# Performance work log

Measured on AMD Instinct MI355X. Metric: run time of the kernel, lower is better.

## Reference

```python
import jax, jax.numpy as jnp
import numpy as np

H = 10          # hidden_size
TAIL = 1440     # slice out[:, -1440:-1, :]


def _cell(x, h, c, w_ih, w_hh, b):
    # PyTorch LSTM gate order: i, f, g, o
    gates = x @ w_ih.T + h @ w_hh.T + b          # [B, 4H]
    i, f, g, o = jnp.split(gates, 4, axis=-1)
    c = jax.nn.sigmoid(f) * c + jax.nn.sigmoid(i) * jnp.tanh(g)
    h = jax.nn.sigmoid(o) * jnp.tanh(c)
    return h, c


def setup_inputs() -> dict:
    key = jax.random.key(0)
    ks = jax.random.split(key, 13)
    s = 1.0 / np.sqrt(H)  # PyTorch default init range

    def u(k, shape):
        return jax.random.uniform(k, shape, jnp.float32, -s, s)

    return {
        "x": jax.random.normal(ks[0], (4096, 2048), jnp.float32),
        "w_ih0": u(ks[1], (4 * H, 1)),
        "w_hh0": u(ks[2], (4 * H, H)),
        "b_ih0": u(ks[3], (4 * H,)),
        "b_hh0": u(ks[4], (4 * H,)),
        "w_ih1": u(ks[5], (4 * H, H)),
        "w_hh1": u(ks[6], (4 * H, H)),
        "b_ih1": u(ks[7], (4 * H,)),
        "b_hh1": u(ks[8], (4 * H,)),
        "fc1_w": u(ks[9], (6, H)),
        "fc1_b": u(ks[10], (6,)),
        "fc2_w": u(ks[11], (1, 6)),
        "fc2_b": u(ks[12], (1,)),
    }


def reference(x, w_ih0, w_hh0, b_ih0, b_hh0, w_ih1, w_hh1, b_ih1, b_hh1,
              fc1_w, fc1_b, fc2_w, fc2_b):
    B, T = x.shape
    xt = x[..., None].transpose(1, 0, 2)         # [T, B, 1] time-major
    b0 = b_ih0 + b_hh0
    b1 = b_ih1 + b_hh1
    z = jnp.zeros((B, H), x.dtype)

    def step(carry, xi):
        h0, c0, h1, c1 = carry
        h0, c0 = _cell(xi, h0, c0, w_ih0, w_hh0, b0)
        h1, c1 = _cell(h0, h1, c1, w_ih1, w_hh1, b1)
        return (h0, c0, h1, c1), h1

    _, ys = jax.lax.scan(step, (z, z, z, z), xt)  # ys: [T, B, H]
    out = ys.transpose(1, 0, 2)[:, T - TAIL:T - 1, :]   # [B, 1439, H]
    out = jnp.tanh(out @ fc1_w.T + fc1_b)                # [B, 1439, 6]
    out = out @ fc2_w.T + fc2_b                          # [B, 1439, 1]
    return out[..., 0]                                   # [B, 1439]
```

## Files before the change

### kernel.cpp

```cpp
#include <hip/hip_runtime.h>

typedef float v2f __attribute__((ext_vector_type(2)));

#define T_LEN 2048
#define NH    10
#define OUT_T 1439
#define TFIRST 608
#define NSEQ  4096
#define CH    16
#define NCH   (T_LEN / CH)
#define MFIRST (TFIRST / CH)

#define KSIG (-1.4426950408889634f)
#define KTAN (-2.8853900817779268f)

static __device__ __forceinline__ v2f fma2(v2f a, v2f b, v2f c) {
  return __builtin_elementwise_fma(a, b, c);
}
static __device__ __forceinline__ v2f splat2(float v) { v2f r; r.x = v; r.y = v; return r; }
static __device__ __forceinline__ v2f mulsp(v2f a, float s) { v2f r; r.x = a.x*s; r.y = a.y*s; return r; }
static __device__ __forceinline__ float rcp1p(float e) {
  return __builtin_amdgcn_rcpf(1.0f + e);
}

#define ROR_F(v, N) __uint_as_float(__builtin_amdgcn_update_dpp( \
    0, (int)__float_as_uint(v), 0x120 + (N), 0xF, 0xF, true))

__global__ void __launch_bounds__(128, 2)
lstm_fused(const float* __restrict__ x,
           const float* __restrict__ w_ih0, const float* __restrict__ w_hh0,
           const float* __restrict__ b_ih0, const float* __restrict__ b_hh0,
           const float* __restrict__ w_ih1, const float* __restrict__ w_hh1,
           const float* __restrict__ b_ih1, const float* __restrict__ b_hh1,
           const float* __restrict__ fc1_w, const float* __restrict__ fc1_b,
           const float* __restrict__ fc2_w, const float* __restrict__ fc2_b,
           float* __restrict__ out)
{
  __shared__ __align__(16) float h0buf[2][CH][64];
  __shared__ __align__(16) float h1buf[2][CH][64];

  const int tid  = threadIdx.x;
  const int wid  = tid >> 6;
  const int lane = tid & 63;
  const int grp  = lane >> 4;
  const int u    = lane & 15;
  const int seq  = (int)blockIdx.x * 4 + grp;

  v2f wIF[NH], wGO[NH], vIF[NH], vGO[NH];
  v2f wx_if, wx_go, bb_if, bb_go;
  wx_if = wx_go = bb_if = bb_go = splat2(0.f);
#pragma unroll
  for (int j = 0; j < NH; ++j) {
    wIF[j] = splat2(0.f); wGO[j] = splat2(0.f);
    vIF[j] = splat2(0.f); vGO[j] = splat2(0.f);
  }
  float fcw[NH];
#pragma unroll
  for (int j = 0; j < NH; ++j) fcw[j] = 0.f;
  float fcb = 0.f, fc2w2 = 0.f, fc2wn = 0.f;
  const float fc2bl = fc2_b[0];

  if (wid == 0) {
    if (u < NH) {
      const int ri = 0*NH+u, rf = 1*NH+u, rg = 2*NH+u, ro = 3*NH+u;
      wx_if.x = KSIG * w_ih0[ri];            wx_if.y = KSIG * w_ih0[rf];
      wx_go.x = KTAN * w_ih0[rg];            wx_go.y = KSIG * w_ih0[ro];
      bb_if.x = KSIG * (b_ih0[ri] + b_hh0[ri]); bb_if.y = KSIG * (b_ih0[rf] + b_hh0[rf]);
      bb_go.x = KTAN * (b_ih0[rg] + b_hh0[rg]); bb_go.y = KSIG * (b_ih0[ro] + b_hh0[ro]);
#pragma unroll
      for (int j = 0; j < NH; ++j) {
        wIF[j].x = KSIG * w_hh0[ri*NH+j]; wIF[j].y = KSIG * w_hh0[rf*NH+j];
        wGO[j].x = KTAN * w_hh0[rg*NH+j]; wGO[j].y = KSIG * w_hh0[ro*NH+j];
      }
    }
    if (u < 6) {
      fcb = KTAN * fc1_b[u];
      const float w2 = fc2_w[u];
      fc2w2 = 2.f * w2; fc2wn = -w2;
#pragma unroll
      for (int j = 0; j < NH; ++j) fcw[j] = KTAN * fc1_w[u*NH + j];
    }
  } else {
    if (u < NH) {
      const int ri = 0*NH+u, rf = 1*NH+u, rg = 2*NH+u, ro = 3*NH+u;
      bb_if.x = KSIG * (b_ih1[ri] + b_hh1[ri]); bb_if.y = KSIG * (b_ih1[rf] + b_hh1[rf]);
      bb_go.x = KTAN * (b_ih1[rg] + b_hh1[rg]); bb_go.y = KSIG * (b_ih1[ro] + b_hh1[ro]);
#pragma unroll
      for (int j = 0; j < NH; ++j) {
        wIF[j].x = KSIG * w_ih1[ri*NH+j]; wIF[j].y = KSIG * w_ih1[rf*NH+j];
        wGO[j].x = KTAN * w_ih1[rg*NH+j]; wGO[j].y = KSIG * w_ih1[ro*NH+j];
        vIF[j].x = KSIG * w_hh1[ri*NH+j]; vIF[j].y = KSIG * w_hh1[rf*NH+j];
        vGO[j].x = KTAN * w_hh1[rg*NH+j]; vGO[j].y = KSIG * w_hh1[ro*NH+j];
      }
    }
  }

  const float* xp   = x + (size_t)seq * T_LEN;
  float*       outp = out + (size_t)seq * OUT_T;

  float c = 0.f;
  float r0=0.f,r1=0.f,r2=0.f,r3=0.f,r4=0.f,r5=0.f,r6=0.f,r7=0.f,r8=0.f,r9=0.f;

  auto a_chunk = [&](int m) {
    float* hb = &h0buf[m & 1][0][0];
    const float* hr = &h0buf[m & 1][0][grp * 16];
    const float4* xq = (const float4*)(xp + m * CH);
    float4 xw[CH / 4];
#pragma unroll
    for (int i = 0; i < CH / 4; ++i) xw[i] = xq[i];
#pragma unroll
    for (int s = 0; s < CH; ++s) {
      const float xv = ((const float*)xw)[s];
      v2f aA = fma2(wx_if, splat2(xv), bb_if);
      v2f gA = fma2(wx_go, splat2(xv), bb_go);
      v2f aB = mulsp(wIF[1], r1);
      v2f gB = mulsp(wGO[1], r1);
#define L0T(j, hv, AC, GC) { const v2f sp = splat2(hv); \
      AC = fma2(wIF[j], sp, AC); GC = fma2(wGO[j], sp, GC); }
      L0T(0,r0,aA,gA) L0T(2,r2,aA,gA) L0T(3,r3,aB,gB) L0T(4,r4,aA,gA)
      L0T(5,r5,aB,gB) L0T(6,r6,aA,gA) L0T(7,r7,aB,gB) L0T(8,r8,aA,gA)
      L0T(9,r9,aB,gB)
#undef L0T
      const v2f gif = aA + aB;
      const v2f ggo = gA + gB;
      const float si = rcp1p(__builtin_amdgcn_exp2f(gif.x));
      const float sf = rcp1p(__builtin_amdgcn_exp2f(gif.y));
      const float rg = rcp1p(__builtin_amdgcn_exp2f(ggo.x));
      const float so = rcp1p(__builtin_amdgcn_exp2f(ggo.y));
      const float tgp = __builtin_fmaf(rg, 2.f*KTAN, -KTAN);
      c = __builtin_fmaf(sf, c, si * tgp);
      const float rc = rcp1p(__builtin_amdgcn_exp2f(c));
      const float tc = __builtin_fmaf(rc, 2.f, -1.f);
      const float h0n = so * tc;
      hb[s*64 + lane] = h0n;
      const float4 va = *(const float4*)(hr + s*64);
      const float4 vb = *(const float4*)(hr + s*64 + 4);
      const float2 vc = *(const float2*)(hr + s*64 + 8);
      r0=va.x; r1=va.y; r2=va.z; r3=va.w;
      r4=vb.x; r5=vb.y; r6=vb.z; r7=vb.w;
      r8=vc.x; r9=vc.y;
    }
  };

  auto b_chunk = [&](int m) {
    const float* hbi = &h0buf[m & 1][0][grp * 16];
    float* ob = &h1buf[m & 1][0][0];
    const float* orr = &h1buf[m & 1][0][grp * 16];
#pragma unroll
    for (int s = 0; s < CH; ++s) {
      const float4 pa = *(const float4*)(hbi + s*64);
      const float4 pb = *(const float4*)(hbi + s*64 + 4);
      const float2 pc = *(const float2*)(hbi + s*64 + 8);
      v2f cA = fma2(wIF[0], splat2(pa.x), bb_if);
      v2f hA = fma2(wGO[0], splat2(pa.x), bb_go);
      v2f cB = mulsp(wIF[1], pa.y);
      v2f hB = mulsp(wGO[1], pa.y);
#define L1I(j, hv, AC, GC) { const v2f sp = splat2(hv); \
      AC = fma2(wIF[j], sp, AC); GC = fma2(wGO[j], sp, GC); }
      L1I(2,pa.z,cA,hA) L1I(3,pa.w,cB,hB) L1I(4,pb.x,cA,hA) L1I(5,pb.y,cB,hB)
      L1I(6,pb.z,cA,hA) L1I(7,pb.w,cB,hB) L1I(8,pc.x,cA,hA) L1I(9,pc.y,cB,hB)
#undef L1I
      v2f cC = mulsp(vIF[0], r0);
      v2f hC = mulsp(vGO[0], r0);
      v2f cD = mulsp(vIF[1], r1);
      v2f hD = mulsp(vGO[1], r1);
#define L1R(j, hv, AC, GC) { const v2f sp = splat2(hv); \
      AC = fma2(vIF[j], sp, AC); GC = fma2(vGO[j], sp, GC); }
      L1R(2,r2,cC,hC) L1R(3,r3,cD,hD) L1R(4,r4,cC,hC) L1R(5,r5,cD,hD)
      L1R(6,r6,cC,hC) L1R(7,r7,cD,hD) L1R(8,r8,cC,hC) L1R(9,r9,cD,hD)
#undef L1R
      const v2f gif = (cA + cB) + (cC + cD);
      const v2f ggo = (hA + hB) + (hC + hD);
      const float si = rcp1p(__builtin_amdgcn_exp2f(gif.x));
      const float sf = rcp1p(__builtin_amdgcn_exp2f(gif.y));
      const float rg = rcp1p(__builtin_amdgcn_exp2f(ggo.x));
      const float so = rcp1p(__builtin_amdgcn_exp2f(ggo.y));
      const float tgp = __builtin_fmaf(rg, 2.f*KTAN, -KTAN);
      c = __builtin_fmaf(sf, c, si * tgp);
      const float rc = rcp1p(__builtin_amdgcn_exp2f(c));
      const float tc = __builtin_fmaf(rc, 2.f, -1.f);
      const float h1n = so * tc;
      ob[s*64 + lane] = h1n;
      const float4 va = *(const float4*)(orr + s*64);
      const float4 vb = *(const float4*)(orr + s*64 + 4);
      const float2 vc = *(const float2*)(orr + s*64 + 8);
      r0=va.x; r1=va.y; r2=va.z; r3=va.w;
      r4=vb.x; r5=vb.y; r6=vb.z; r7=vb.w;
      r8=vc.x; r9=vc.y;
    }
  };

  auto fc_chunk = [&](int m) {
    const float* hb = &h1buf[m & 1][0][grp * 16];
    float* oq = outp + (m * CH - TFIRST);
#pragma unroll
    for (int s = 0; s < CH; ++s) {
      if (m * CH + s < TFIRST + OUT_T) {
        const float4 pa = *(const float4*)(hb + s*64);
        const float4 pb = *(const float4*)(hb + s*64 + 4);
        const float2 pc = *(const float2*)(hb + s*64 + 8);
        float acc = __builtin_fmaf(pa.x, fcw[0], fcb);
        acc = __builtin_fmaf(pa.y, fcw[1], acc);
        acc = __builtin_fmaf(pa.z, fcw[2], acc);
        acc = __builtin_fmaf(pa.w, fcw[3], acc);
        acc = __builtin_fmaf(pb.x, fcw[4], acc);
        acc = __builtin_fmaf(pb.y, fcw[5], acc);
        acc = __builtin_fmaf(pb.z, fcw[6], acc);
        acc = __builtin_fmaf(pb.w, fcw[7], acc);
        acc = __builtin_fmaf(pc.x, fcw[8], acc);
        acc = __builtin_fmaf(pc.y, fcw[9], acc);
        const float rc = rcp1p(__builtin_amdgcn_exp2f(acc));
        float y = __builtin_fmaf(rc, fc2w2, fc2wn);
        y += ROR_F(y, 8);
        y += ROR_F(y, 4);
        y += ROR_F(y, 2);
        y += ROR_F(y, 1);
        if (u == 0) oq[s] = y + fc2bl;
      }
    }
  };

#pragma unroll 1
  for (int r = 0; r < NCH + 2; ++r) {
    if (wid == 0) {
      if (r < NCH) a_chunk(r);
      const int m = r - 2;
      if (m >= MFIRST && m < NCH) fc_chunk(m);
    } else {
      if (r >= 1 && r <= NCH) b_chunk(r - 1);
    }
    __syncthreads();
  }
}

extern "C" void kernel_launch(void* const* d_in, const int* in_sizes, int n_in,
                              void* d_out, int out_size, void* d_ws, size_t ws_size,
                              hipStream_t stream) {
  const float* x     = (const float*)d_in[0];
  const float* w_ih0 = (const float*)d_in[1];
  const float* w_hh0 = (const float*)d_in[2];
  const float* b_ih0 = (const float*)d_in[3];
  const float* b_hh0 = (const float*)d_in[4];
  const float* w_ih1 = (const float*)d_in[5];
  const float* w_hh1 = (const float*)d_in[6];
  const float* b_ih1 = (const float*)d_in[7];
  const float* b_hh1 = (const float*)d_in[8];
  const float* fc1_w = (const float*)d_in[9];
  const float* fc1_b = (const float*)d_in[10];
  const float* fc2_w = (const float*)d_in[11];
  const float* fc2_b = (const float*)d_in[12];
  float* out = (float*)d_out;

  lstm_fused<<<dim3(NSEQ / 4), dim3(128), 0, stream>>>(
      x, w_ih0, w_hh0, b_ih0, b_hh0, w_ih1, w_hh1, b_ih1, b_hh1,
      fc1_w, fc1_b, fc2_w, fc2_b, out);
}
```

Before: 724.0 us.

## Broadcast recurrent hidden state via ds_swizzle, double chunk size, partially unroll

Within each recurrent step, the new hidden values are now broadcast across the lanes of each 16-lane group with ds_swizzle broadcasts, replacing the previous write-then-read through shared memory. Chunk length doubles from 16 to 32 steps, halving the number of block-wide barriers. Loops change from full unroll to 4-step bodies to keep code size and registers in check. The risk is that ten swizzles per step may cost as much as the LDS reads, and the reduced unrolling may hurt scheduling.

```diff
diff --git a/kernel.cpp b/kernel.cpp
--- a/kernel.cpp
+++ b/kernel.cpp
@@ -7,7 +7,7 @@
 #define OUT_T 1439
 #define TFIRST 608
 #define NSEQ  4096
-#define CH    16
+#define CH    32
 #define NCH   (T_LEN / CH)
 #define MFIRST (TFIRST / CH)
 
@@ -22,6 +22,9 @@
 static __device__ __forceinline__ float rcp1p(float e) {
   return __builtin_amdgcn_rcpf(1.0f + e);
 }
+
+#define SWZB(v, j) __uint_as_float(__builtin_amdgcn_ds_swizzle( \
+    (int)__float_as_uint(v), (((j) << 5) | 0x10)))
 
 #define ROR_F(v, N) __uint_as_float(__builtin_amdgcn_update_dpp( \
     0, (int)__float_as_uint(v), 0x120 + (N), 0xF, 0xF, true))
@@ -101,121 +104,133 @@
   float c = 0.f;
   float r0=0.f,r1=0.f,r2=0.f,r3=0.f,r4=0.f,r5=0.f,r6=0.f,r7=0.f,r8=0.f,r9=0.f;
 
+  auto l0_step = [&](float xv, float* dst) {
+    v2f aA = fma2(wx_if, splat2(xv), bb_if);
+    v2f gA = fma2(wx_go, splat2(xv), bb_go);
+    v2f aB = mulsp(wIF[1], r1);
+    v2f gB = mulsp(wGO[1], r1);
+#define L0T(j, hv) { const v2f sp = splat2(hv); \
+    ((j & 1) ? aB : aA) = fma2(wIF[j], sp, ((j & 1) ? aB : aA)); \
+    ((j & 1) ? gB : gA) = fma2(wGO[j], sp, ((j & 1) ? gB : gA)); }
+    L0T(0,r0) L0T(2,r2) L0T(3,r3) L0T(4,r4) L0T(5,r5)
+    L0T(6,r6) L0T(7,r7) L0T(8,r8) L0T(9,r9)
+#undef L0T
+    const v2f gif = aA + aB;
+    const v2f ggo = gA + gB;
+    const float si = rcp1p(__builtin_amdgcn_exp2f(gif.x));
+    const float sf = rcp1p(__builtin_amdgcn_exp2f(gif.y));
+    const float rg = rcp1p(__builtin_amdgcn_exp2f(ggo.x));
+    const float so = rcp1p(__builtin_amdgcn_exp2f(ggo.y));
+    const float tgp = __builtin_fmaf(rg, 2.f*KTAN, -KTAN);
+    c = __builtin_fmaf(sf, c, si * tgp);
+    const float rc = rcp1p(__builtin_amdgcn_exp2f(c));
+    const float tc = __builtin_fmaf(rc, 2.f, -1.f);
+    const float h0n = so * tc;
+    *dst = h0n;
+    r0 = SWZB(h0n,0); r1 = SWZB(h0n,1); r2 = SWZB(h0n,2); r3 = SWZB(h0n,3);
+    r4 = SWZB(h0n,4); r5 = SWZB(h0n,5); r6 = SWZB(h0n,6); r7 = SWZB(h0n,7);
+    r8 = SWZB(h0n,8); r9 = SWZB(h0n,9);
+  };
+
   auto a_chunk = [&](int m) {
-    float* hb = &h0buf[m & 1][0][0];
-    const float* hr = &h0buf[m & 1][0][grp * 16];
+    float* hb = &h0buf[m & 1][0][0] + lane;
     const float4* xq = (const float4*)(xp + m * CH);
-    float4 xw[CH / 4];
-#pragma unroll
-    for (int i = 0; i < CH / 4; ++i) xw[i] = xq[i];
-#pragma unroll
-    for (int s = 0; s < CH; ++s) {
-      const float xv = ((const float*)xw)[s];
-      v2f aA = fma2(wx_if, splat2(xv), bb_if);
-      v2f gA = fma2(wx_go, splat2(xv), bb_go);
-      v2f aB = mulsp(wIF[1], r1);
-      v2f gB = mulsp(wGO[1], r1);
-#define L0T(j, hv, AC, GC) { const v2f sp = splat2(hv); \
-      AC = fma2(wIF[j], sp, AC); GC = fma2(wGO[j], sp, GC); }
-      L0T(0,r0,aA,gA) L0T(2,r2,aA,gA) L0T(3,r3,aB,gB) L0T(4,r4,aA,gA)
-      L0T(5,r5,aB,gB) L0T(6,r6,aA,gA) L0T(7,r7,aB,gB) L0T(8,r8,aA,gA)
-      L0T(9,r9,aB,gB)
-#undef L0T
-      const v2f gif = aA + aB;
-      const v2f ggo = gA + gB;
-      const float si = rcp1p(__builtin_amdgcn_exp2f(gif.x));
-      const float sf = rcp1p(__builtin_amdgcn_exp2f(gif.y));
-      const float rg = rcp1p(__builtin_amdgcn_exp2f(ggo.x));
-      const float so = rcp1p(__builtin_amdgcn_exp2f(ggo.y));
-      const float tgp = __builtin_fmaf(rg, 2.f*KTAN, -KTAN);
-      c = __builtin_fmaf(sf, c, si * tgp);
-      const float rc = rcp1p(__builtin_amdgcn_exp2f(c));
-      const float tc = __builtin_fmaf(rc, 2.f, -1.f);
-      const float h0n = so * tc;
-      hb[s*64 + lane] = h0n;
-      const float4 va = *(const float4*)(hr + s*64);
-      const float4 vb = *(const float4*)(hr + s*64 + 4);
-      const float2 vc = *(const float2*)(hr + s*64 + 8);
-      r0=va.x; r1=va.y; r2=va.z; r3=va.w;
-      r4=vb.x; r5=vb.y; r6=vb.z; r7=vb.w;
-      r8=vc.x; r9=vc.y;
-    }
+#pragma unroll 1
+    for (int b = 0; b < CH / 4; ++b) {
+      const float4 xb = xq[b];
+      float* d = hb + b * 256;
+      l0_step(xb.x, d);
+      l0_step(xb.y, d + 64);
+      l0_step(xb.z, d + 128);
+      l0_step(xb.w, d + 192);
+    }
+  };
+
+  auto l1_step = [&](const float* hp, float* dst) {
+    const float4 pa = *(const float4*)(hp);
+    const float4 pb = *(const float4*)(hp + 4);
+    const float2 pc = *(const float2*)(hp + 8);
+    v2f cA = fma2(wIF[0], splat2(pa.x), bb_if);
+    v2f hA = fma2(wGO[0], splat2(pa.x), bb_go);
+    v2f cB = mulsp(wIF[1], pa.y);
+    v2f hB = mulsp(wGO[1], pa.y);
+#define L1I(j, hv, AC, GC) { const v2f sp = splat2(hv); \
+    AC = fma2(wIF[j], sp, AC); GC = fma2(wGO[j], sp, GC); }
+    L1I(2,pa.z,cA,hA) L1I(3,pa.w,cB,hB) L1I(4,pb.x,cA,hA) L1I(5,pb.y,cB,hB)
+    L1I(6,pb.z,cA,hA) L1I(7,pb.w,cB,hB) L1I(8,pc.x,cA,hA) L1I(9,pc.y,cB,hB)
+#undef L1I
+    v2f cC = mulsp(vIF[0], r0);
+    v2f hC = mulsp(vGO[0], r0);
+    v2f cD = mulsp(vIF[1], r1);
+    v2f hD = mulsp(vGO[1], r1);
+#define L1R(j, hv, AC, GC) { const v2f sp = splat2(hv); \
+    AC = fma2(vIF[j], sp, AC); GC = fma2(vGO[j], sp, GC); }
+    L1R(2,r2,cC,hC) L1R(3,r3,cD,hD) L1R(4,r4,cC,hC) L1R(5,r5,cD,hD)
+    L1R(6,r6,cC,hC) L1R(7,r7,cD,hD) L1R(8,r8,cC,hC) L1R(9,r9,cD,hD)
+#undef L1R
+    const v2f gif = (cA + cB) + (cC + cD);
+    const v2f ggo = (hA + hB) + (hC + hD);
+    const float si = rcp1p(__builtin_amdgcn_exp2f(gif.x));
+    const float sf = rcp1p(__builtin_amdgcn_exp2f(gif.y));
+    const float rg = rcp1p(__builtin_amdgcn_exp2f(ggo.x));
+    const float so = rcp1p(__builtin_amdgcn_exp2f(ggo.y));
+    const float tgp = __builtin_fmaf(rg, 2.f*KTAN, -KTAN);
+    c = __builtin_fmaf(sf, c, si * tgp);
+    const float rc = rcp1p(__builtin_amdgcn_exp2f(c));
+    const float tc = __builtin_fmaf(rc, 2.f, -1.f);
+    const float h1n = so * tc;
+    *dst = h1n;
+    r0 = SWZB(h1n,0); r1 = SWZB(h1n,1); r2 = SWZB(h1n,2); r3 = SWZB(h1n,3);
+    r4 = SWZB(h1n,4); r5 = SWZB(h1n,5); r6 = SWZB(h1n,6); r7 = SWZB(h1n,7);
+    r8 = SWZB(h1n,8); r9 = SWZB(h1n,9);
   };
 
   auto b_chunk = [&](int m) {
     const float* hbi = &h0buf[m & 1][0][grp * 16];
-    float* ob = &h1buf[m & 1][0][0];
-    const float* orr = &h1buf[m & 1][0][grp * 16];
-#pragma unroll
-    for (int s = 0; s < CH; ++s) {
-      const float4 pa = *(const float4*)(hbi + s*64);
-      const float4 pb = *(const float4*)(hbi + s*64 + 4);
-      const float2 pc = *(const float2*)(hbi + s*64 + 8);
-      v2f cA = fma2(wIF[0], splat2(pa.x), bb_if);
-      v2f hA = fma2(wGO[0], splat2(pa.x), bb_go);
-      v2f cB = mulsp(wIF[1], pa.y);
-      v2f hB = mulsp(wGO[1], pa.y);
-#define L1I(j, hv, AC, GC) { const v2f sp = splat2(hv); \
-      AC = fma2(wIF[j], sp, AC); GC = fma2(wGO[j], sp, GC); }
-      L1I(2,pa.z,cA,hA) L1I(3,pa.w,cB,hB) L1I(4,pb.x,cA,hA) L1I(5,pb.y,cB,hB)
-      L1I(6,pb.z,cA,hA) L1I(7,pb.w,cB,hB) L1I(8,pc.x,cA,hA) L1I(9,pc.y,cB,hB)
-#undef L1I
-      v2f cC = mulsp(vIF[0], r0);
-      v2f hC = mulsp(vGO[0], r0);
-      v2f cD = mulsp(vIF[1], r1);
-      v2f hD = mulsp(vGO[1], r1);
-#define L1R(j, hv, AC, GC) { const v2f sp = splat2(hv); \
-      AC = fma2(vIF[j], sp, AC); GC = fma2(vGO[j], sp, GC); }
-      L1R(2,r2,cC,hC) L1R(3,r3,cD,hD) L1R(4,r4,cC,hC) L1R(5,r5,cD,hD)
-      L1R(6,r6,cC,hC) L1R(7,r7,cD,hD) L1R(8,r8,cC,hC) L1R(9,r9,cD,hD)
-#undef L1R
-      const v2f gif = (cA + cB) + (cC + cD);
-      const v2f ggo = (hA + hB) + (hC + hD);
-      const float si = rcp1p(__builtin_amdgcn_exp2f(gif.x));
-      const float sf = rcp1p(__builtin_amdgcn_exp2f(gif.y));
-      const float rg = rcp1p(__builtin_amdgcn_exp2f(ggo.x));
-      const float so = rcp1p(__builtin_amdgcn_exp2f(ggo.y));
-      const float tgp = __builtin_fmaf(rg, 2.f*KTAN, -KTAN);
-      c = __builtin_fmaf(sf, c, si * tgp);
-      const float rc = rcp1p(__builtin_amdgcn_exp2f(c));
-      const float tc = __builtin_fmaf(rc, 2.f, -1.f);
-      const float h1n = so * tc;
-      ob[s*64 + lane] = h1n;
-      const float4 va = *(const float4*)(orr + s*64);
-      const float4 vb = *(const float4*)(orr + s*64 + 4);
-      const float2 vc = *(const float2*)(orr + s*64 + 8);
-      r0=va.x; r1=va.y; r2=va.z; r3=va.w;
-      r4=vb.x; r5=vb.y; r6=vb.z; r7=vb.w;
-      r8=vc.x; r9=vc.y;
+    float* ob = &h1buf[m & 1][0][0] + lane;
+#pragma unroll 1
+    for (int b = 0; b < CH / 4; ++b) {
+      const float* hp = hbi + b * 256;
+      float* d = ob + b * 256;
+      l1_step(hp,       d);
+      l1_step(hp + 64,  d + 64);
+      l1_step(hp + 128, d + 128);
+      l1_step(hp + 192, d + 192);
     }
   };
 
   auto fc_chunk = [&](int m) {
     const float* hb = &h1buf[m & 1][0][grp * 16];
     float* oq = outp + (m * CH - TFIRST);
-#pragma unroll
-    for (int s = 0; s < CH; ++s) {
-      if (m * CH + s < TFIRST + OUT_T) {
-        const float4 pa = *(const float4*)(hb + s*64);
-        const float4 pb = *(const float4*)(hb + s*64 + 4);
-        const float2 pc = *(const float2*)(hb + s*64 + 8);
-        float acc = __builtin_fmaf(pa.x, fcw[0], fcb);
-        acc = __builtin_fmaf(pa.y, fcw[1], acc);
-        acc = __builtin_fmaf(pa.z, fcw[2], acc);
-        acc = __builtin_fmaf(pa.w, fcw[3], acc);
-        acc = __builtin_fmaf(pb.x, fcw[4], acc);
-        acc = __builtin_fmaf(pb.y, fcw[5], acc);
-        acc = __builtin_fmaf(pb.z, fcw[6], acc);
-        acc = __builtin_fmaf(pb.w, fcw[7], acc);
-        acc = __builtin_fmaf(pc.x, fcw[8], acc);
-        acc = __builtin_fmaf(pc.y, fcw[9], acc);
-        const float rc = rcp1p(__builtin_amdgcn_exp2f(acc));
-        float y = __builtin_fmaf(rc, fc2w2, fc2wn);
-        y += ROR_F(y, 8);
-        y += ROR_F(y, 4);
-        y += ROR_F(y, 2);
-        y += ROR_F(y, 1);
-        if (u == 0) oq[s] = y + fc2bl;
+    const int tbase = m * CH;
+#pragma unroll 1
+    for (int b = 0; b < CH / 4; ++b) {
+      const float* hp = hb + b * 256;
+#pragma unroll
+      for (int k = 0; k < 4; ++k) {
+        const int s = b * 4 + k;
+        if (tbase + s < TFIRST + OUT_T) {
+          const float4 pa = *(const float4*)(hp + k*64);
+          const float4 pb = *(const float4*)(hp + k*64 + 4);
+          const float2 pc = *(const float2*)(hp + k*64 + 8);
+          float acc = __builtin_fmaf(pa.x, fcw[0], fcb);
+          acc = __builtin_fmaf(pa.y, fcw[1], acc);
+          acc = __builtin_fmaf(pa.z, fcw[2], acc);
+          acc = __builtin_fmaf(pa.w, fcw[3], acc);
+          acc = __builtin_fmaf(pb.x, fcw[4], acc);
+          acc = __builtin_fmaf(pb.y, fcw[5], acc);
+          acc = __builtin_fmaf(pb.z, fcw[6], acc);
+          acc = __builtin_fmaf(pb.w, fcw[7], acc);
+          acc = __builtin_fmaf(pc.x, fcw[8], acc);
+          acc = __builtin_fmaf(pc.y, fcw[9], acc);
+          const float rc = rcp1p(__builtin_amdgcn_exp2f(acc));
+          float y = __builtin_fmaf(rc, fc2w2, fc2wn);
+          y += ROR_F(y, 8);
+          y += ROR_F(y, 4);
+          y += ROR_F(y, 2);
+          y += ROR_F(y, 1);
+          if (u == 0) oq[s] = y + fc2bl;
+        }
       }
     }
   };
```

New measurement: 753.4 us. 4.1% more time.

## Exchange recurrent hidden state via DPP rotates and fold FC head into spare lanes

Applied to the files above, without the earlier changes.

Each lane's recurrent weights are pre-rotated so the 16-lane group can gather neighbouring h values with DPP row rotates. This replaces the per-step LDS store and reload of the recurrent hidden state, which sat on the serial critical path. The separate h1 buffer and the fc_chunk pass on the layer-0 wave are removed. The FC head is computed by lanes 10-15 of the layer-1 wave, using their otherwise idle g-gate slot on the previous step's h1, and the output index is shifted by one to match. The cost is 15 DPP ops and more FMAs per step, since the recurrent loop now runs over 16 slots instead of 10, plus higher register pressure.

```diff
diff --git a/kernel.cpp b/kernel.cpp
--- a/kernel.cpp
+++ b/kernel.cpp
@@ -9,7 +9,6 @@
 #define NSEQ  4096
 #define CH    16
 #define NCH   (T_LEN / CH)
-#define MFIRST (TFIRST / CH)
 
 #define KSIG (-1.4426950408889634f)
 #define KTAN (-2.8853900817779268f)
@@ -37,7 +36,6 @@
            float* __restrict__ out)
 {
   __shared__ __align__(16) float h0buf[2][CH][64];
-  __shared__ __align__(16) float h1buf[2][CH][64];
 
   const int tid  = threadIdx.x;
   const int wid  = tid >> 6;
@@ -46,18 +44,14 @@
   const int u    = lane & 15;
   const int seq  = (int)blockIdx.x * 4 + grp;
 
-  v2f wIF[NH], wGO[NH], vIF[NH], vGO[NH];
+  v2f wRif[16], wRgo[16], wIF[NH], wGO[NH];
   v2f wx_if, wx_go, bb_if, bb_go;
   wx_if = wx_go = bb_if = bb_go = splat2(0.f);
 #pragma unroll
-  for (int j = 0; j < NH; ++j) {
-    wIF[j] = splat2(0.f); wGO[j] = splat2(0.f);
-    vIF[j] = splat2(0.f); vGO[j] = splat2(0.f);
-  }
-  float fcw[NH];
-#pragma unroll
-  for (int j = 0; j < NH; ++j) fcw[j] = 0.f;
-  float fcb = 0.f, fc2w2 = 0.f, fc2wn = 0.f;
+  for (int k = 0; k < 16; ++k) { wRif[k] = splat2(0.f); wRgo[k] = splat2(0.f); }
+#pragma unroll
+  for (int j = 0; j < NH; ++j) { wIF[j] = splat2(0.f); wGO[j] = splat2(0.f); }
+  float fc2s = 0.f;
   const float fc2bl = fc2_b[0];
 
   if (wid == 0) {
@@ -68,17 +62,13 @@
       bb_if.x = KSIG * (b_ih0[ri] + b_hh0[ri]); bb_if.y = KSIG * (b_ih0[rf] + b_hh0[rf]);
       bb_go.x = KTAN * (b_ih0[rg] + b_hh0[rg]); bb_go.y = KSIG * (b_ih0[ro] + b_hh0[ro]);
 #pragma unroll
-      for (int j = 0; j < NH; ++j) {
-        wIF[j].x = KSIG * w_hh0[ri*NH+j]; wIF[j].y = KSIG * w_hh0[rf*NH+j];
-        wGO[j].x = KTAN * w_hh0[rg*NH+j]; wGO[j].y = KSIG * w_hh0[ro*NH+j];
-      }
-    }
-    if (u < 6) {
-      fcb = KTAN * fc1_b[u];
-      const float w2 = fc2_w[u];
-      fc2w2 = 2.f * w2; fc2wn = -w2;
-#pragma unroll
-      for (int j = 0; j < NH; ++j) fcw[j] = KTAN * fc1_w[u*NH + j];
+      for (int k = 0; k < 16; ++k) {
+        const int j = (u - k) & 15;
+        if (j < NH) {
+          wRif[k].x = KSIG * w_hh0[ri*NH+j]; wRif[k].y = KSIG * w_hh0[rf*NH+j];
+          wRgo[k].x = KTAN * w_hh0[rg*NH+j]; wRgo[k].y = KSIG * w_hh0[ro*NH+j];
+        }
+      }
     }
   } else {
     if (u < NH) {
@@ -89,8 +79,23 @@
       for (int j = 0; j < NH; ++j) {
         wIF[j].x = KSIG * w_ih1[ri*NH+j]; wIF[j].y = KSIG * w_ih1[rf*NH+j];
         wGO[j].x = KTAN * w_ih1[rg*NH+j]; wGO[j].y = KSIG * w_ih1[ro*NH+j];
-        vIF[j].x = KSIG * w_hh1[ri*NH+j]; vIF[j].y = KSIG * w_hh1[rf*NH+j];
-        vGO[j].x = KTAN * w_hh1[rg*NH+j]; vGO[j].y = KSIG * w_hh1[ro*NH+j];
+      }
+#pragma unroll
+      for (int k = 0; k < 16; ++k) {
+        const int j = (u - k) & 15;
+        if (j < NH) {
+          wRif[k].x = KSIG * w_hh1[ri*NH+j]; wRif[k].y = KSIG * w_hh1[rf*NH+j];
+          wRgo[k].x = KTAN * w_hh1[rg*NH+j]; wRgo[k].y = KSIG * w_hh1[ro*NH+j];
+        }
+      }
+    } else {
+      const int p = u - NH;
+      bb_go.x = KTAN * fc1_b[p];
+      fc2s = fc2_w[p] / KTAN;
+#pragma unroll
+      for (int k = 0; k < 16; ++k) {
+        const int j = (u - k) & 15;
+        if (j < NH) wRgo[k].x = KTAN * fc1_w[p*NH + j];
       }
     }
   }
@@ -99,135 +104,101 @@
   float*       outp = out + (size_t)seq * OUT_T;
 
   float c = 0.f;
-  float r0=0.f,r1=0.f,r2=0.f,r3=0.f,r4=0.f,r5=0.f,r6=0.f,r7=0.f,r8=0.f,r9=0.f;
+  float h = 0.f;
+
+#define RK(K, AIF, AGO) { const float hk = ROR_F(h, K); const v2f sp = splat2(hk); \
+    AIF = fma2(wRif[K], sp, AIF); AGO = fma2(wRgo[K], sp, AGO); }
+
+  auto l0_step = [&](float xv, float* dst) {
+    v2f aA = fma2(wx_if, splat2(xv), bb_if);
+    v2f gA = fma2(wx_go, splat2(xv), bb_go);
+    { const v2f sp = splat2(h); aA = fma2(wRif[0], sp, aA); gA = fma2(wRgo[0], sp, gA); }
+    const float h1r = ROR_F(h, 1);
+    v2f aB = mulsp(wRif[1], h1r);
+    v2f gB = mulsp(wRgo[1], h1r);
+    RK(2,aA,gA)  RK(3,aB,gB)  RK(4,aA,gA)  RK(5,aB,gB)
+    RK(6,aA,gA)  RK(7,aB,gB)  RK(8,aA,gA)  RK(9,aB,gB)
+    RK(10,aA,gA) RK(11,aB,gB) RK(12,aA,gA) RK(13,aB,gB)
+    RK(14,aA,gA) RK(15,aB,gB)
+    const v2f gif = aA + aB;
+    const v2f ggo = gA + gB;
+    const float si = rcp1p(__builtin_amdgcn_exp2f(gif.x));
+    const float sf = rcp1p(__builtin_amdgcn_exp2f(gif.y));
+    const float rg = rcp1p(__builtin_amdgcn_exp2f(ggo.x));
+    const float so = rcp1p(__builtin_amdgcn_exp2f(ggo.y));
+    const float tgp = __builtin_fmaf(rg, 2.f*KTAN, -KTAN);
+    c = __builtin_fmaf(sf, c, si * tgp);
+    const float rc = rcp1p(__builtin_amdgcn_exp2f(c));
+    const float tc = __builtin_fmaf(rc, 2.f, -1.f);
+    h = so * tc;
+    *dst = h;
+  };
 
   auto a_chunk = [&](int m) {
-    float* hb = &h0buf[m & 1][0][0];
-    const float* hr = &h0buf[m & 1][0][grp * 16];
+    float* hb = &h0buf[m & 1][0][0] + lane;
     const float4* xq = (const float4*)(xp + m * CH);
     float4 xw[CH / 4];
 #pragma unroll
     for (int i = 0; i < CH / 4; ++i) xw[i] = xq[i];
 #pragma unroll
-    for (int s = 0; s < CH; ++s) {
-      const float xv = ((const float*)xw)[s];
-      v2f aA = fma2(wx_if, splat2(xv), bb_if);
-      v2f gA = fma2(wx_go, splat2(xv), bb_go);
-      v2f aB = mulsp(wIF[1], r1);
-      v2f gB = mulsp(wGO[1], r1);
-#define L0T(j, hv, AC, GC) { const v2f sp = splat2(hv); \
-      AC = fma2(wIF[j], sp, AC); GC = fma2(wGO[j], sp, GC); }
-      L0T(0,r0,aA,gA) L0T(2,r2,aA,gA) L0T(3,r3,aB,gB) L0T(4,r4,aA,gA)
-      L0T(5,r5,aB,gB) L0T(6,r6,aA,gA) L0T(7,r7,aB,gB) L0T(8,r8,aA,gA)
-      L0T(9,r9,aB,gB)
-#undef L0T
-      const v2f gif = aA + aB;
-      const v2f ggo = gA + gB;
-      const float si = rcp1p(__builtin_amdgcn_exp2f(gif.x));
-      const float sf = rcp1p(__builtin_amdgcn_exp2f(gif.y));
-      const float rg = rcp1p(__builtin_amdgcn_exp2f(ggo.x));
-      const float so = rcp1p(__builtin_amdgcn_exp2f(ggo.y));
-      const float tgp = __builtin_fmaf(rg, 2.f*KTAN, -KTAN);
-      c = __builtin_fmaf(sf, c, si * tgp);
-      const float rc = rcp1p(__builtin_amdgcn_exp2f(c));
-      const float tc = __builtin_fmaf(rc, 2.f, -1.f);
-      const float h0n = so * tc;
-      hb[s*64 + lane] = h0n;
-      const float4 va = *(const float4*)(hr + s*64);
-      const float4 vb = *(const float4*)(hr + s*64 + 4);
-      const float2 vc = *(const float2*)(hr + s*64 + 8);
-      r0=va.x; r1=va.y; r2=va.z; r3=va.w;
-      r4=vb.x; r5=vb.y; r6=vb.z; r7=vb.w;
-      r8=vc.x; r9=vc.y;
+    for (int s = 0; s < CH; ++s) l0_step(((const float*)xw)[s], hb + s * 64);
+  };
+
+  auto l1_step = [&](const float* hp, float* optr, bool do_out) {
+    const float4 pa = *(const float4*)(hp);
+    const float4 pb = *(const float4*)(hp + 4);
+    const float2 pc = *(const float2*)(hp + 8);
+    v2f cA = fma2(wIF[0], splat2(pa.x), bb_if);
+    v2f hA = fma2(wGO[0], splat2(pa.x), bb_go);
+    v2f cB = mulsp(wIF[1], pa.y);
+    v2f hB = mulsp(wGO[1], pa.y);
+#define L1I(j, hv, AC, GC) { const v2f sp = splat2(hv); \
+    AC = fma2(wIF[j], sp, AC); GC = fma2(wGO[j], sp, GC); }
+    L1I(2,pa.z,cA,hA) L1I(3,pa.w,cB,hB) L1I(4,pb.x,cA,hA) L1I(5,pb.y,cB,hB)
+    L1I(6,pb.z,cA,hA) L1I(7,pb.w,cB,hB) L1I(8,pc.x,cA,hA) L1I(9,pc.y,cB,hB)
+#undef L1I
+    { const v2f sp = splat2(h); cA = fma2(wRif[0], sp, cA); hA = fma2(wRgo[0], sp, hA); }
+    RK(1,cB,hB)  RK(2,cA,hA)  RK(3,cB,hB)  RK(4,cA,hA)
+    RK(5,cB,hB)  RK(6,cA,hA)  RK(7,cB,hB)  RK(8,cA,hA)
+    RK(9,cB,hB)  RK(10,cA,hA) RK(11,cB,hB) RK(12,cA,hA)
+    RK(13,cB,hB) RK(14,cA,hA) RK(15,cB,hB)
+    const v2f gif = cA + cB;
+    const v2f ggo = hA + hB;
+    const float si = rcp1p(__builtin_amdgcn_exp2f(gif.x));
+    const float sf = rcp1p(__builtin_amdgcn_exp2f(gif.y));
+    const float rg = rcp1p(__builtin_amdgcn_exp2f(ggo.x));
+    const float so = rcp1p(__builtin_amdgcn_exp2f(ggo.y));
+    const float tgp = __builtin_fmaf(rg, 2.f*KTAN, -KTAN);
+    c = __builtin_fmaf(sf, c, si * tgp);
+    const float rc = rcp1p(__builtin_amdgcn_exp2f(c));
+    const float tc = __builtin_fmaf(rc, 2.f, -1.f);
+    h = so * tc;
+    if (do_out) {
+      float y = tgp * fc2s;
+      y += ROR_F(y, 8);
+      y += ROR_F(y, 4);
+      y += ROR_F(y, 2);
+      y += ROR_F(y, 1);
+      if (u == 0) *optr = y + fc2bl;
     }
   };
 
   auto b_chunk = [&](int m) {
     const float* hbi = &h0buf[m & 1][0][grp * 16];
-    float* ob = &h1buf[m & 1][0][0];
-    const float* orr = &h1buf[m & 1][0][grp * 16];
-#pragma unroll
-    for (int s = 0; s < CH; ++s) {
-      const float4 pa = *(const float4*)(hbi + s*64);
-      const float4 pb = *(const float4*)(hbi + s*64 + 4);
-      const float2 pc = *(const float2*)(hbi + s*64 + 8);
-      v2f cA = fma2(wIF[0], splat2(pa.x), bb_if);
-      v2f hA = fma2(wGO[0], splat2(pa.x), bb_go);
-      v2f cB = mulsp(wIF[1], pa.y);
-      v2f hB = mulsp(wGO[1], pa.y);
-#define L1I(j, hv, AC, GC) { const v2f sp = splat2(hv); \
-      AC = fma2(wIF[j], sp, AC); GC = fma2(wGO[j], sp, GC); }
-      L1I(2,pa.z,cA,hA) L1I(3,pa.w,cB,hB) L1I(4,pb.x,cA,hA) L1I(5,pb.y,cB,hB)
-      L1I(6,pb.z,cA,hA) L1I(7,pb.w,cB,hB) L1I(8,pc.x,cA,hA) L1I(9,pc.y,cB,hB)
-#undef L1I
-      v2f cC = mulsp(vIF[0], r0);
-      v2f hC = mulsp(vGO[0], r0);
-      v2f cD = mulsp(vIF[1], r1);
-      v2f hD = mulsp(vGO[1], r1);
-#define L1R(j, hv, AC, GC) { const v2f sp = splat2(hv); \
-      AC = fma2(vIF[j], sp, AC); GC = fma2(vGO[j], sp, GC); }
-      L1R(2,r2,cC,hC) L1R(3,r3,cD,hD) L1R(4,r4,cC,hC) L1R(5,r5,cD,hD)
-      L1R(6,r6,cC,hC) L1R(7,r7,cD,hD) L1R(8,r8,cC,hC) L1R(9,r9,cD,hD)
-#undef L1R
-      const v2f gif = (cA + cB) + (cC + cD);
-      const v2f ggo = (hA + hB) + (hC + hD);
-      const float si = rcp1p(__builtin_amdgcn_exp2f(gif.x));
-      const float sf = rcp1p(__builtin_amdgcn_exp2f(gif.y));
-      const float rg = rcp1p(__builtin_amdgcn_exp2f(ggo.x));
-      const float so = rcp1p(__builtin_amdgcn_exp2f(ggo.y));
-      const float tgp = __builtin_fmaf(rg, 2.f*KTAN, -KTAN);
-      c = __builtin_fmaf(sf, c, si * tgp);
-      const float rc = rcp1p(__builtin_amdgcn_exp2f(c));
-      const float tc = __builtin_fmaf(rc, 2.f, -1.f);
-      const float h1n = so * tc;
-      ob[s*64 + lane] = h1n;
-      const float4 va = *(const float4*)(orr + s*64);
-      const float4 vb = *(const float4*)(orr + s*64 + 4);
-      const float2 vc = *(const float2*)(orr + s*64 + 8);
-      r0=va.x; r1=va.y; r2=va.z; r3=va.w;
-      r4=vb.x; r5=vb.y; r6=vb.z; r7=vb.w;
-      r8=vc.x; r9=vc.y;
-    }
-  };
-
-  auto fc_chunk = [&](int m) {
-    const float* hb = &h1buf[m & 1][0][grp * 16];
-    float* oq = outp + (m * CH - TFIRST);
-#pragma unroll
-    for (int s = 0; s < CH; ++s) {
-      if (m * CH + s < TFIRST + OUT_T) {
-        const float4 pa = *(const float4*)(hb + s*64);
-        const float4 pb = *(const float4*)(hb + s*64 + 4);
-        const float2 pc = *(const float2*)(hb + s*64 + 8);
-        float acc = __builtin_fmaf(pa.x, fcw[0], fcb);
-        acc = __builtin_fmaf(pa.y, fcw[1], acc);
-        acc = __builtin_fmaf(pa.z, fcw[2], acc);
-        acc = __builtin_fmaf(pa.w, fcw[3], acc);
-        acc = __builtin_fmaf(pb.x, fcw[4], acc);
-        acc = __builtin_fmaf(pb.y, fcw[5], acc);
-        acc = __builtin_fmaf(pb.z, fcw[6], acc);
-        acc = __builtin_fmaf(pb.w, fcw[7], acc);
-        acc = __builtin_fmaf(pc.x, fcw[8], acc);
-        acc = __builtin_fmaf(pc.y, fcw[9], acc);
-        const float rc = rcp1p(__builtin_amdgcn_exp2f(acc));
-        float y = __builtin_fmaf(rc, fc2w2, fc2wn);
-        y += ROR_F(y, 8);
-        y += ROR_F(y, 4);
-        y += ROR_F(y, 2);
-        y += ROR_F(y, 1);
-        if (u == 0) oq[s] = y + fc2bl;
-      }
-    }
-  };
+    const int tbase = m * CH;
+    float* oq = outp + (tbase - 1 - TFIRST);
+#pragma unroll
+    for (int s = 0; s < CH; ++s)
+      l1_step(hbi + s * 64, oq + s, tbase + s > TFIRST);
+  };
+#undef RK
 
 #pragma unroll 1
-  for (int r = 0; r < NCH + 2; ++r) {
+  for (int r = 0; r < NCH + 1; ++r) {
     if (wid == 0) {
       if (r < NCH) a_chunk(r);
-      const int m = r - 2;
-      if (m >= MFIRST && m < NCH) fc_chunk(m);
     } else {
-      if (r >= 1 && r <= NCH) b_chunk(r - 1);
+      if (r >= 1) b_chunk(r - 1);
     }
     __syncthreads();
   }
```

Measured after the change: 934.4 us. +29.1%, slower.
